# Kernel tuning notes

Hardware: AMD Instinct MI355X
Metric: run time of the kernel (lower is better)

Reference implementation:

```python
import jax, jax.numpy as jnp
import numpy as np

EPS_BN = 1e-5
EPS_NORM = 1e-12


def _l2norm_c(x):
    # F.normalize over channel dim (dim=1) of [n, d, h, w]
    n = jnp.sqrt(jnp.sum(x * x, axis=1, keepdims=True))
    return x / jnp.maximum(n, EPS_NORM)


def setup_inputs() -> dict:
    key = jax.random.key(0)
    ks = jax.random.split(key, 8)
    g, p, d, h, w = 64, 64, 512, 24, 8
    hw = h * w
    return {
        "gal_fea": jax.random.normal(ks[0], (g, d, h, w), dtype=jnp.float32),
        "prob_fea": jax.random.normal(ks[1], (p, d, h, w), dtype=jnp.float32),
        "bn_weight": jax.random.uniform(ks[2], (1,), dtype=jnp.float32) + 0.5,
        "bn_bias": jax.random.uniform(ks[3], (1,), dtype=jnp.float32) - 0.5,
        "bn_mean": jnp.zeros((1,), dtype=jnp.float32),
        "bn_var": jnp.ones((1,), dtype=jnp.float32),
        "fc_weight": jax.random.normal(ks[4], (1, 2 * hw), dtype=jnp.float32) * 0.05,
        "fc_bias": jax.random.normal(ks[5], (1,), dtype=jnp.float32) * 0.05,
        "lbn_weight": jax.random.uniform(ks[6], (1,), dtype=jnp.float32) + 0.5,
        "lbn_bias": jax.random.uniform(ks[7], (1,), dtype=jnp.float32) - 0.5,
        "lbn_mean": jnp.zeros((1,), dtype=jnp.float32),
        "lbn_var": jnp.ones((1,), dtype=jnp.float32),
    }


def reference(gal_fea, prob_fea, bn_weight, bn_bias, bn_mean, bn_var,
              fc_weight, fc_bias, lbn_weight, lbn_bias, lbn_mean, lbn_var):
    g, d, h, w = gal_fea.shape
    p = prob_fea.shape[0]
    hw = h * w

    # L2-normalize over channels, flatten spatial dims
    gal = _l2norm_c(gal_fea).reshape(g, d, hw)              # [g, d, j]
    ker = _l2norm_c(prob_fea).transpose(0, 2, 3, 1).reshape(p, hw, d)  # [p, i, d]

    # cosine-similarity cross-correlation: s[g,p,i,j] = <probe pos i, gallery pos j>
    s = jnp.einsum('pid,gdj->gpij', ker, gal)               # [g, p, hw, hw]

    # dual spatial max-pool: max over probe positions, max over gallery positions
    score = jnp.concatenate([s.max(axis=2), s.max(axis=3)], axis=-1)  # [g, p, 2*hw]

    # eval-mode BatchNorm1d(1): scalar affine broadcast over all elements
    score = (score - bn_mean) / jnp.sqrt(bn_var + EPS_BN) * bn_weight + bn_bias

    # fc: Linear(2*hw, 1)
    score = jnp.einsum('gpk,ok->gpo', score, fc_weight)[..., 0] + fc_bias[0]  # [g, p]

    # eval-mode logit BatchNorm1d(1): scalar affine
    score = (score - lbn_mean) / jnp.sqrt(lbn_var + EPS_BN) * lbn_weight + lbn_bias

    return jax.nn.sigmoid(score / 10.0)
```

## Files before the change

### kernel.cpp

```cpp
#include <hip/hip_runtime.h>

#define HW 192
#define DD 512
#define GG 64
#define PP 64
#define SLAB 98304

typedef __attribute__((ext_vector_type(4))) int intx4;

__device__ __forceinline__ unsigned int pk4(float a, float b, float c, float d) {
  int qa = (int)rintf(a), qb = (int)rintf(b), qc = (int)rintf(c), qd = (int)rintf(d);
  return (unsigned)(qa & 255) | ((unsigned)(qb & 255) << 8) |
         ((unsigned)(qc & 255) << 16) | ((unsigned)(qd & 255) << 24);
}

__global__ __launch_bounds__(512, 2) void norm_kernel(
    const float* __restrict__ gal, const float* __restrict__ prob,
    unsigned char* __restrict__ ws) {
  int b = blockIdx.x;
  int s = b / 12;
  int q = b - s * 12;
  const float* in = (s < GG) ? (gal + (size_t)s * DD * HW)
                             : (prob + (size_t)(s - GG) * DD * HW);
  unsigned char* out = ws + (size_t)s * SLAB;
  int pos0 = q * 16;
  int t = threadIdx.x;

  __shared__ float T[16][524];
  __shared__ float sqa[128][17];
  __shared__ float sq2[16][17];
  __shared__ float scl[16];

  {
    int cq = t >> 2;
    int quad = t & 3;
    float p0 = 0.f, p1 = 0.f, p2 = 0.f, p3 = 0.f;
#pragma unroll
    for (int cb = 0; cb < 4; ++cb) {
      int c = cb * 128 + cq;
      const float4 v = *(const float4*)(in + (size_t)c * HW + pos0 + quad * 4);
      T[quad * 4 + 0][c] = v.x;
      T[quad * 4 + 1][c] = v.y;
      T[quad * 4 + 2][c] = v.z;
      T[quad * 4 + 3][c] = v.w;
      p0 += v.x * v.x; p1 += v.y * v.y; p2 += v.z * v.z; p3 += v.w * v.w;
    }
    sqa[cq][quad * 4 + 0] = p0;
    sqa[cq][quad * 4 + 1] = p1;
    sqa[cq][quad * 4 + 2] = p2;
    sqa[cq][quad * 4 + 3] = p3;
  }
  __syncthreads();
  if (t < 256) {
    int g2 = t >> 4, pos = t & 15;
    float v = 0.f;
#pragma unroll
    for (int r = 0; r < 8; ++r) v += sqa[g2 * 8 + r][pos];
    sq2[g2][pos] = v;
  }
  __syncthreads();
  if (t < 16) {
    float v = 0.f;
#pragma unroll
    for (int r = 0; r < 16; ++r) v += sq2[r][t];
    scl[t] = 1.f / fmaxf(sqrtf(v), 1e-12f);
  }
  __syncthreads();

  {
    int kb2 = t >> 6;
    int lane = t & 63;
    int l4 = lane >> 4;
    int pos = lane & 15;
    float sc = scl[pos] * 127.f;
    int base = kb2 * 64 + l4 * 16;
    const float4 r0 = *(const float4*)&T[pos][base + 0];
    const float4 r1 = *(const float4*)&T[pos][base + 4];
    const float4 r2 = *(const float4*)&T[pos][base + 8];
    const float4 r3 = *(const float4*)&T[pos][base + 12];
    uint4 u;
    u.x = pk4(r0.x * sc, r0.y * sc, r0.z * sc, r0.w * sc);
    u.y = pk4(r1.x * sc, r1.y * sc, r1.z * sc, r1.w * sc);
    u.z = pk4(r2.x * sc, r2.y * sc, r2.z * sc, r2.w * sc);
    u.w = pk4(r3.x * sc, r3.y * sc, r3.z * sc, r3.w * sc);
    *(uint4*)(out + (size_t)kb2 * 12288 + (size_t)q * 1024 + (size_t)lane * 16) = u;
  }
}

#define GLOAD_LDS16(gp, lp)                                              \
  __builtin_amdgcn_global_load_lds(                                      \
      (const __attribute__((address_space(1))) unsigned int*)(gp),       \
      (__attribute__((address_space(3))) unsigned int*)(lp), 16, 0, 0)

__global__ __launch_bounds__(256, 2) void qaconv_gemm(
    const unsigned char* __restrict__ ws, const float* __restrict__ fcw,
    const float* __restrict__ bnw, const float* __restrict__ bnb,
    const float* __restrict__ bnm, const float* __restrict__ bnv,
    const float* __restrict__ fcb, const float* __restrict__ lw,
    const float* __restrict__ lb, const float* __restrict__ lm,
    const float* __restrict__ lv, float* __restrict__ out) {
  int bid0 = blockIdx.x;
  int bid = ((bid0 & 7) << 9) + (bid0 >> 3);
  int sb = bid >> 6, li = bid & 63;
  int g = ((sb >> 3) << 3) + (li >> 3);
  int p = ((sb & 7) << 3) + (li & 7);
  const unsigned char* Bsrc = ws + (size_t)g * SLAB;
  const unsigned char* Asrc = ws + (size_t)(GG + p) * SLAB;

  __shared__ unsigned char sbuf[2][24576];

  int tid = threadIdx.x;
  int lane = tid & 63;
  int wave = tid >> 6;
  int wi = wave >> 1, wj = wave & 1;
  int l15 = lane & 15, l4 = lane >> 4;

  intx4 acc[6][6];
#pragma unroll
  for (int a = 0; a < 6; ++a)
#pragma unroll
    for (int c = 0; c < 6; ++c) acc[a][c] = (intx4){0, 0, 0, 0};

  const unsigned char* stgsrc =
      ((wave < 2) ? Asrc : Bsrc) + (size_t)((wave & 1) * 6) * 1024 +
      (size_t)lane * 16;
  int fbase = wave * 6;

#define STAGE(BUF, KB)                                                    \
  do {                                                                    \
    const unsigned char* s_ = stgsrc + (size_t)(KB)*12288;                \
    _Pragma("unroll") for (int i_ = 0; i_ < 6; ++i_) {                    \
      GLOAD_LDS16(s_ + i_ * 1024, &sbuf[BUF][(fbase + i_) * 1024]);       \
    }                                                                     \
  } while (0)

  intx4 aR[2][6], bR[2][6];

#define DSRD(RB, KB)                                                      \
  do {                                                                    \
    const unsigned char* cb_ = &sbuf[(KB)&1][lane * 16];                  \
    _Pragma("unroll") for (int i_ = 0; i_ < 6; ++i_) {                    \
      aR[RB][i_] = *(const intx4*)(cb_ + (wi * 6 + i_) * 1024);           \
      bR[RB][i_] = *(const intx4*)(cb_ + (12 + wj * 6 + i_) * 1024);      \
    }                                                                     \
  } while (0)

  STAGE(0, 0);
  __syncthreads();
  DSRD(0, 0);
  STAGE(1, 1);

#pragma unroll
  for (int kb = 0; kb < 8; ++kb) {
    __syncthreads();
    if (kb < 6) STAGE(kb & 1, kb + 2);
    if (kb < 7) DSRD((kb + 1) & 1, kb + 1);
#pragma unroll
    for (int jt = 0; jt < 6; ++jt) {
      intx4 bb = bR[kb & 1][jt];
#pragma unroll
      for (int it = 0; it < 6; ++it)
        acc[it][jt] = __builtin_amdgcn_mfma_i32_16x16x64_i8(
            aR[kb & 1][it], bb, acc[it][jt], 0, 0, 0);
    }
  }
#undef STAGE
#undef DSRD

  __syncthreads();

  float (*colpart)[HW] = (float (*)[HW]) & sbuf[0][0];
  float (*rowpart)[HW] = (float (*)[HW]) & sbuf[0][1536];
  float (*redbuf)[2] = (float (*)[2]) & sbuf[0][3072];

  const float inv = 1.f / 16129.f;
  int cm[6];
  int rm[6][4];
#pragma unroll
  for (int jt = 0; jt < 6; ++jt) cm[jt] = -2147483647;
#pragma unroll
  for (int it = 0; it < 6; ++it)
#pragma unroll
    for (int r = 0; r < 4; ++r) rm[it][r] = -2147483647;
#pragma unroll
  for (int it = 0; it < 6; ++it)
#pragma unroll
    for (int jt = 0; jt < 6; ++jt)
#pragma unroll
      for (int r = 0; r < 4; ++r) {
        int v = acc[it][jt][r];
        cm[jt] = max(cm[jt], v);
        rm[it][r] = max(rm[it][r], v);
      }

#pragma unroll
  for (int jt = 0; jt < 6; ++jt) {
    int v = cm[jt];
    v = max(v, __shfl_xor(v, 16, 64));
    v = max(v, __shfl_xor(v, 32, 64));
    if (lane < 16) colpart[wi][wj * 96 + jt * 16 + lane] = (float)v * inv;
  }
#pragma unroll
  for (int it = 0; it < 6; ++it)
#pragma unroll
    for (int r = 0; r < 4; ++r) {
      int v = rm[it][r];
      v = max(v, __shfl_xor(v, 1, 64));
      v = max(v, __shfl_xor(v, 2, 64));
      v = max(v, __shfl_xor(v, 4, 64));
      v = max(v, __shfl_xor(v, 8, 64));
      if (l15 == 0) rowpart[wj][wi * 96 + it * 16 + l4 * 4 + r] = (float)v * inv;
    }
  __syncthreads();

  float part = 0.f, wpart = 0.f;
  if (tid < HW) {
    float cmax = fmaxf(colpart[0][tid], colpart[1][tid]);
    float rmax = fmaxf(rowpart[0][tid], rowpart[1][tid]);
    float w1 = fcw[tid], w2 = fcw[HW + tid];
    part = cmax * w1 + rmax * w2;
    wpart = w1 + w2;
  }
#pragma unroll
  for (int off = 32; off > 0; off >>= 1) {
    part += __shfl_down(part, off, 64);
    wpart += __shfl_down(wpart, off, 64);
  }
  if (lane == 0) { redbuf[wave][0] = part; redbuf[wave][1] = wpart; }
  __syncthreads();
  if (tid == 0) {
    float s = redbuf[0][0] + redbuf[1][0] + redbuf[2][0] + redbuf[3][0];
    float wsum = redbuf[0][1] + redbuf[1][1] + redbuf[2][1] + redbuf[3][1];
    float bnA = bnw[0] * rsqrtf(bnv[0] + 1e-5f);
    float bnB = bnb[0] - bnm[0] * bnA;
    float sc = bnA * s + bnB * wsum + fcb[0];
    float lA = lw[0] * rsqrtf(lv[0] + 1e-5f);
    sc = (sc - lm[0]) * lA + lb[0];
    out[g * PP + p] = 1.f / (1.f + __expf(-sc * 0.1f));
  }
}

extern "C" void kernel_launch(void* const* d_in, const int* in_sizes, int n_in,
                              void* d_out, int out_size, void* d_ws, size_t ws_size,
                              hipStream_t stream) {
  const float* gal  = (const float*)d_in[0];
  const float* prob = (const float*)d_in[1];
  const float* bnw  = (const float*)d_in[2];
  const float* bnb  = (const float*)d_in[3];
  const float* bnm  = (const float*)d_in[4];
  const float* bnv  = (const float*)d_in[5];
  const float* fcw  = (const float*)d_in[6];
  const float* fcb  = (const float*)d_in[7];
  const float* lw   = (const float*)d_in[8];
  const float* lb   = (const float*)d_in[9];
  const float* lm   = (const float*)d_in[10];
  const float* lv   = (const float*)d_in[11];
  unsigned char* ws = (unsigned char*)d_ws;
  float* out = (float*)d_out;

  hipLaunchKernelGGL(norm_kernel, dim3(1536), dim3(512), 0, stream, gal, prob, ws);
  hipLaunchKernelGGL(qaconv_gemm, dim3(GG * PP), dim3(256), 0, stream, ws, fcw,
                     bnw, bnb, bnm, bnv, fcb, lw, lb, lm, lv, out);
}
```

Measured before the change: 205.8 us.

## Switch int8 GEMM to 32x32x32 MFMA with four-slot slice pipeline and new layout

Replaces the 16x16x64 int8 MFMA tiling (6x6 tiles per wave) with 32x32x32 MFMA (3x3 tiles of 16 accumulators each). The normalize kernel writes quantized data in a new K-slice layout that matches the 32x32 operand fragment, and the GEMM stages half-size slices into a four-buffer LDS ring so two slices are in flight. This aims to cut LDS reads and MFMA issue count per FLOP and improve load/compute overlap. The epilogue row and column max reductions are rewritten for the 32x32 accumulator layout, and any mismatch in the index mapping would produce wrong results.

Measured after the change: 242.8 us. 1.18x slower.

```diff
diff --git a/kernel.cpp b/kernel.cpp
--- a/kernel.cpp
+++ b/kernel.cpp
@@ -7,6 +7,7 @@
 #define SLAB 98304
 
 typedef __attribute__((ext_vector_type(4))) int intx4;
+typedef __attribute__((ext_vector_type(16))) int intx16;
 
 __device__ __forceinline__ unsigned int pk4(float a, float b, float c, float d) {
   int qa = (int)rintf(a), qb = (int)rintf(b), qc = (int)rintf(c), qd = (int)rintf(d);
@@ -68,22 +69,23 @@
   __syncthreads();
 
   {
-    int kb2 = t >> 6;
-    int lane = t & 63;
-    int l4 = lane >> 4;
-    int pos = lane & 15;
-    float sc = scl[pos] * 127.f;
-    int base = kb2 * 64 + l4 * 16;
-    const float4 r0 = *(const float4*)&T[pos][base + 0];
-    const float4 r1 = *(const float4*)&T[pos][base + 4];
-    const float4 r2 = *(const float4*)&T[pos][base + 8];
-    const float4 r3 = *(const float4*)&T[pos][base + 12];
+    int p15 = t & 15;
+    int m = t >> 4;
+    float sc = scl[p15] * 127.f;
+    int base = m * 16;
+    const float4 r0 = *(const float4*)&T[p15][base + 0];
+    const float4 r1 = *(const float4*)&T[p15][base + 4];
+    const float4 r2 = *(const float4*)&T[p15][base + 8];
+    const float4 r3 = *(const float4*)&T[p15][base + 12];
     uint4 u;
     u.x = pk4(r0.x * sc, r0.y * sc, r0.z * sc, r0.w * sc);
     u.y = pk4(r1.x * sc, r1.y * sc, r1.z * sc, r1.w * sc);
     u.z = pk4(r2.x * sc, r2.y * sc, r2.z * sc, r2.w * sc);
     u.w = pk4(r3.x * sc, r3.y * sc, r3.z * sc, r3.w * sc);
-    *(uint4*)(out + (size_t)kb2 * 12288 + (size_t)q * 1024 + (size_t)lane * 16) = u;
+    int S = m >> 1;
+    int rt = q >> 1;
+    int fl = p15 + ((q & 1) << 4) + ((m & 1) << 5);
+    *(uint4*)(out + (size_t)S * 6144 + (size_t)rt * 1024 + (size_t)fl * 16) = u;
   }
 }
 
@@ -107,65 +109,79 @@
   const unsigned char* Bsrc = ws + (size_t)g * SLAB;
   const unsigned char* Asrc = ws + (size_t)(GG + p) * SLAB;
 
-  __shared__ unsigned char sbuf[2][24576];
+  __shared__ unsigned char sbuf[4][12288];
 
   int tid = threadIdx.x;
   int lane = tid & 63;
   int wave = tid >> 6;
   int wi = wave >> 1, wj = wave & 1;
-  int l15 = lane & 15, l4 = lane >> 4;
-
-  intx4 acc[6][6];
-#pragma unroll
-  for (int a = 0; a < 6; ++a)
-#pragma unroll
-    for (int c = 0; c < 6; ++c) acc[a][c] = (intx4){0, 0, 0, 0};
-
-  const unsigned char* stgsrc =
-      ((wave < 2) ? Asrc : Bsrc) + (size_t)((wave & 1) * 6) * 1024 +
-      (size_t)lane * 16;
-  int fbase = wave * 6;
-
-#define STAGE(BUF, KB)                                                    \
+
+  intx16 acc[3][3];
+#pragma unroll
+  for (int a = 0; a < 3; ++a)
+#pragma unroll
+    for (int c = 0; c < 3; ++c)
+#pragma unroll
+      for (int r = 0; r < 16; ++r) acc[a][c][r] = 0;
+
+  int sab = wave & 1;
+  int sidx = wave >> 1;
+  const unsigned char* stgbase =
+      (sab ? Bsrc : Asrc) + (size_t)lane * 16;
+
+#define STAGE_SLICE(S)                                                    \
   do {                                                                    \
-    const unsigned char* s_ = stgsrc + (size_t)(KB)*12288;                \
-    _Pragma("unroll") for (int i_ = 0; i_ < 6; ++i_) {                    \
-      GLOAD_LDS16(s_ + i_ * 1024, &sbuf[BUF][(fbase + i_) * 1024]);       \
+    const unsigned char* s_ = stgbase + (size_t)(S)*6144;                 \
+    _Pragma("unroll") for (int r_ = 0; r_ < 6; ++r_) {                    \
+      GLOAD_LDS16(s_ + r_ * 1024,                                         \
+                  &sbuf[(S) & 3][sab * 6144 + r_ * 1024]);                \
     }                                                                     \
   } while (0)
 
-  intx4 aR[2][6], bR[2][6];
-
-#define DSRD(RB, KB)                                                      \
+#define DSRD(S, AX, BX)                                                   \
   do {                                                                    \
-    const unsigned char* cb_ = &sbuf[(KB)&1][lane * 16];                  \
-    _Pragma("unroll") for (int i_ = 0; i_ < 6; ++i_) {                    \
-      aR[RB][i_] = *(const intx4*)(cb_ + (wi * 6 + i_) * 1024);           \
-      bR[RB][i_] = *(const intx4*)(cb_ + (12 + wj * 6 + i_) * 1024);      \
+    const unsigned char* c_ = &sbuf[(S) & 3][lane * 16];                  \
+    _Pragma("unroll") for (int i_ = 0; i_ < 3; ++i_) {                    \
+      AX[i_] = *(const intx4*)(c_ + (wi * 3 + i_) * 1024);                \
+      BX[i_] = *(const intx4*)(c_ + 6144 + (wj * 3 + i_) * 1024);         \
     }                                                                     \
   } while (0)
 
-  STAGE(0, 0);
-  __syncthreads();
-  DSRD(0, 0);
-  STAGE(1, 1);
+#define MFMA9(AX, BX)                                                     \
+  do {                                                                    \
+    _Pragma("unroll") for (int tj_ = 0; tj_ < 3; ++tj_) {                 \
+      intx4 bb = BX[tj_];                                                 \
+      _Pragma("unroll") for (int ti_ = 0; ti_ < 3; ++ti_)                 \
+          acc[ti_][tj_] = __builtin_amdgcn_mfma_i32_32x32x32_i8(          \
+              AX[ti_], bb, acc[ti_][tj_], 0, 0, 0);                       \
+    }                                                                     \
+  } while (0)
+
+  intx4 a0[3], b0[3], a1[3], b1[3];
+
+  {
+    int S = sidx;
+    STAGE_SLICE(S);
+  }
+  if (sidx == 0) STAGE_SLICE(2);
+  __syncthreads();
+  DSRD(0, a0, b0);
 
 #pragma unroll
   for (int kb = 0; kb < 8; ++kb) {
     __syncthreads();
-    if (kb < 6) STAGE(kb & 1, kb + 2);
-    if (kb < 7) DSRD((kb + 1) & 1, kb + 1);
-#pragma unroll
-    for (int jt = 0; jt < 6; ++jt) {
-      intx4 bb = bR[kb & 1][jt];
-#pragma unroll
-      for (int it = 0; it < 6; ++it)
-        acc[it][jt] = __builtin_amdgcn_mfma_i32_16x16x64_i8(
-            aR[kb & 1][it], bb, acc[it][jt], 0, 0, 0);
+    {
+      int S = 2 * kb + 3 + sidx;
+      if (S <= 15) STAGE_SLICE(S);
     }
-  }
-#undef STAGE
+    DSRD(2 * kb + 1, a1, b1);
+    MFMA9(a0, b0);
+    if (kb < 7) DSRD(2 * kb + 2, a0, b0);
+    MFMA9(a1, b1);
+  }
+#undef STAGE_SLICE
 #undef DSRD
+#undef MFMA9
 
   __syncthreads();
 
@@ -174,42 +190,44 @@
   float (*redbuf)[2] = (float (*)[2]) & sbuf[0][3072];
 
   const float inv = 1.f / 16129.f;
-  int cm[6];
-  int rm[6][4];
-#pragma unroll
-  for (int jt = 0; jt < 6; ++jt) cm[jt] = -2147483647;
-#pragma unroll
-  for (int it = 0; it < 6; ++it)
-#pragma unroll
-    for (int r = 0; r < 4; ++r) rm[it][r] = -2147483647;
-#pragma unroll
-  for (int it = 0; it < 6; ++it)
-#pragma unroll
-    for (int jt = 0; jt < 6; ++jt)
-#pragma unroll
-      for (int r = 0; r < 4; ++r) {
-        int v = acc[it][jt][r];
-        cm[jt] = max(cm[jt], v);
-        rm[it][r] = max(rm[it][r], v);
+  int cm[3];
+  int rm[3][16];
+#pragma unroll
+  for (int tj = 0; tj < 3; ++tj) cm[tj] = -2147483647;
+#pragma unroll
+  for (int ti = 0; ti < 3; ++ti)
+#pragma unroll
+    for (int r = 0; r < 16; ++r) rm[ti][r] = -2147483647;
+#pragma unroll
+  for (int ti = 0; ti < 3; ++ti)
+#pragma unroll
+    for (int tj = 0; tj < 3; ++tj)
+#pragma unroll
+      for (int r = 0; r < 16; ++r) {
+        int v = acc[ti][tj][r];
+        cm[tj] = max(cm[tj], v);
+        rm[ti][r] = max(rm[ti][r], v);
       }
 
 #pragma unroll
-  for (int jt = 0; jt < 6; ++jt) {
-    int v = cm[jt];
-    v = max(v, __shfl_xor(v, 16, 64));
+  for (int tj = 0; tj < 3; ++tj) {
+    int v = cm[tj];
     v = max(v, __shfl_xor(v, 32, 64));
-    if (lane < 16) colpart[wi][wj * 96 + jt * 16 + lane] = (float)v * inv;
-  }
-#pragma unroll
-  for (int it = 0; it < 6; ++it)
-#pragma unroll
-    for (int r = 0; r < 4; ++r) {
-      int v = rm[it][r];
+    if (lane < 32) colpart[wi][wj * 96 + tj * 32 + lane] = (float)v * inv;
+  }
+#pragma unroll
+  for (int ti = 0; ti < 3; ++ti)
+#pragma unroll
+    for (int r = 0; r < 16; ++r) {
+      int v = rm[ti][r];
       v = max(v, __shfl_xor(v, 1, 64));
       v = max(v, __shfl_xor(v, 2, 64));
       v = max(v, __shfl_xor(v, 4, 64));
       v = max(v, __shfl_xor(v, 8, 64));
-      if (l15 == 0) rowpart[wj][wi * 96 + it * 16 + l4 * 4 + r] = (float)v * inv;
+      v = max(v, __shfl_xor(v, 16, 64));
+      if ((lane & 31) == 0)
+        rowpart[wj][wi * 96 + ti * 32 + (r & 3) + 8 * (r >> 2) +
+                    4 * (lane >> 5)] = (float)v * inv;
     }
   __syncthreads();
 
```

## Triple-buffer LDS staging with explicit vmcnt waits and MFMA priority

Applied to the files above, without the earlier changes.

Moves the int8 GEMM main loop from a double-buffered LDS ring to a triple-buffered one, with two K-blocks of global-to-LDS loads in flight. The full __syncthreads drain is replaced by partial s_waitcnt vmcnt counts plus a raw barrier, so later stages keep loading while the current block computes. MFMA sections run at raised wave priority via s_setprio. This adds 24KB of LDS per block, which may lower occupancy, and the hand-counted vmcnt values must match the number of outstanding loads or the reads become incorrect.

Result: slower. 212.0 us (+3.0%).

```diff
diff --git a/kernel.cpp b/kernel.cpp
--- a/kernel.cpp
+++ b/kernel.cpp
@@ -107,7 +107,7 @@
   const unsigned char* Bsrc = ws + (size_t)g * SLAB;
   const unsigned char* Asrc = ws + (size_t)(GG + p) * SLAB;
 
-  __shared__ unsigned char sbuf[2][24576];
+  __shared__ unsigned char sbuf[3][24576];
 
   int tid = threadIdx.x;
   int lane = tid & 63;
@@ -126,46 +126,66 @@
       (size_t)lane * 16;
   int fbase = wave * 6;
 
-#define STAGE(BUF, KB)                                                    \
+#define STAGE(KB)                                                         \
   do {                                                                    \
     const unsigned char* s_ = stgsrc + (size_t)(KB)*12288;                \
     _Pragma("unroll") for (int i_ = 0; i_ < 6; ++i_) {                    \
-      GLOAD_LDS16(s_ + i_ * 1024, &sbuf[BUF][(fbase + i_) * 1024]);       \
+      GLOAD_LDS16(s_ + i_ * 1024, &sbuf[(KB) % 3][(fbase + i_) * 1024]);  \
     }                                                                     \
   } while (0)
 
   intx4 aR[2][6], bR[2][6];
 
-#define DSRD(RB, KB)                                                      \
-  do {                                                                    \
-    const unsigned char* cb_ = &sbuf[(KB)&1][lane * 16];                  \
+#define DSRD(KB, RB)                                                      \
+  do {                                                                    \
+    const unsigned char* cb_ = &sbuf[(KB) % 3][lane * 16];                \
     _Pragma("unroll") for (int i_ = 0; i_ < 6; ++i_) {                    \
       aR[RB][i_] = *(const intx4*)(cb_ + (wi * 6 + i_) * 1024);           \
       bR[RB][i_] = *(const intx4*)(cb_ + (12 + wj * 6 + i_) * 1024);      \
     }                                                                     \
   } while (0)
 
-  STAGE(0, 0);
-  __syncthreads();
+#define MFMAB(RB)                                                         \
+  do {                                                                    \
+    _Pragma("unroll") for (int jt_ = 0; jt_ < 6; ++jt_) {                 \
+      intx4 bb = bR[RB][jt_];                                             \
+      _Pragma("unroll") for (int it_ = 0; it_ < 6; ++it_)                 \
+          acc[it_][jt_] = __builtin_amdgcn_mfma_i32_16x16x64_i8(          \
+              aR[RB][it_], bb, acc[it_][jt_], 0, 0, 0);                   \
+    }                                                                     \
+  } while (0)
+
+#define PHASE(KB, VMW)                                                    \
+  do {                                                                    \
+    asm volatile("s_waitcnt vmcnt(" #VMW ") lgkmcnt(0)" ::: "memory");    \
+    __builtin_amdgcn_s_barrier();                                         \
+    if ((KB) + 3 <= 7) STAGE((KB) + 3);                                   \
+    if ((KB) + 1 <= 7) DSRD((KB) + 1, ((KB) + 1) & 1);                    \
+    __builtin_amdgcn_s_setprio(1);                                        \
+    MFMAB((KB)&1);                                                        \
+    __builtin_amdgcn_s_setprio(0);                                        \
+  } while (0)
+
+  STAGE(0);
+  STAGE(1);
+  STAGE(2);
+  asm volatile("s_waitcnt vmcnt(12)" ::: "memory");
+  __builtin_amdgcn_s_barrier();
   DSRD(0, 0);
-  STAGE(1, 1);
-
-#pragma unroll
-  for (int kb = 0; kb < 8; ++kb) {
-    __syncthreads();
-    if (kb < 6) STAGE(kb & 1, kb + 2);
-    if (kb < 7) DSRD((kb + 1) & 1, kb + 1);
-#pragma unroll
-    for (int jt = 0; jt < 6; ++jt) {
-      intx4 bb = bR[kb & 1][jt];
-#pragma unroll
-      for (int it = 0; it < 6; ++it)
-        acc[it][jt] = __builtin_amdgcn_mfma_i32_16x16x64_i8(
-            aR[kb & 1][it], bb, acc[it][jt], 0, 0, 0);
-    }
-  }
+
+  PHASE(0, 6);
+  PHASE(1, 6);
+  PHASE(2, 6);
+  PHASE(3, 6);
+  PHASE(4, 6);
+  PHASE(5, 6);
+  PHASE(6, 0);
+  PHASE(7, 0);
+
 #undef STAGE
 #undef DSRD
+#undef MFMAB
+#undef PHASE
 
   __syncthreads();
 
```
